# Kernel tuning notes

Hardware: AMD Instinct MI355X
Metric: run time of the kernel (lower is better)

## Reference

```python
import jax, jax.numpy as jnp
import numpy as np
import math

B, N, DIM = 2, 4096, 256
NUM_HEADS = 8
HEAD_DIM = DIM // NUM_HEADS
WINDOW = 7  # default window_size in create_local_mask


def local_mask(seq_len: int, window_size: int = WINDOW) -> jnp.ndarray:
    """Boolean [N,N] mask: True where attention is allowed (2D grid locality)."""
    grid = int(math.isqrt(seq_len))
    idx = jnp.arange(seq_len)
    row, col = idx // grid, idx % grid
    half = window_size // 2
    ok_row = jnp.abs(row[:, None] - row[None, :]) <= half
    ok_col = jnp.abs(col[:, None] - col[None, :]) <= half
    return ok_row & ok_col


def setup_inputs() -> dict:
    key = jax.random.key(0)
    k1, k2, k3, k4 = jax.random.split(key, 4)
    x = jax.random.normal(k1, (B, N, DIM), dtype=jnp.float32)
    W_qkv = jax.random.normal(k2, (3 * DIM, DIM), dtype=jnp.float32) * (DIM ** -0.5)
    W_proj = jax.random.normal(k3, (DIM, DIM), dtype=jnp.float32) * (DIM ** -0.5)
    b_proj = jax.random.normal(k4, (DIM,), dtype=jnp.float32) * 0.01
    temperature = jnp.ones((1,), dtype=jnp.float32)
    return {"x": x, "W_qkv": W_qkv, "W_proj": W_proj, "b_proj": b_proj,
            "temperature": temperature}


def reference(x, W_qkv, W_proj, b_proj, temperature):
    Bb, Nn, C = x.shape
    scale = HEAD_DIM ** -0.5
    # qkv linear (no bias): [B,N,3C] -> [3,B,H,N,hd]
    qkv = (x @ W_qkv.T).reshape(Bb, Nn, 3, NUM_HEADS, HEAD_DIM)
    qkv = jnp.transpose(qkv, (2, 0, 3, 1, 4))
    q, k, v = qkv[0], qkv[1], qkv[2]
    # scores with learnable temperature
    attn = jnp.einsum('bhqd,bhkd->bhqk', q, k) * (scale * temperature[0])
    mask = local_mask(Nn)  # training path: N > 100 -> mask applied
    attn = jnp.where(mask[None, None, :, :], attn, -jnp.inf)
    attn = jax.nn.softmax(attn, axis=-1)
    out = jnp.einsum('bhqk,bhkd->bhqd', attn, v)  # [B,H,N,hd]
    out = jnp.transpose(out, (0, 2, 1, 3)).reshape(Bb, Nn, C)
    return out @ W_proj.T + b_proj
```

## Files before the change

### kernel.cpp

```cpp
#include <hip/hip_runtime.h>
#include <hip/hip_bf16.h>
#include <hip/hip_fp16.h>
#include <math.h>

#define DIM   256
#define NHEAD 8
#define HD    32
#define NTOK  4096
#define GRD   64
#define BATCH 2
#define MTOT  (BATCH * NTOK)

typedef __attribute__((ext_vector_type(8))) short bf16x8;
typedef __attribute__((ext_vector_type(4))) float f32x4;
typedef _Float16 h8 __attribute__((ext_vector_type(8)));
typedef _Float16 h2v __attribute__((ext_vector_type(2)));

#if defined(__has_builtin)
#if __has_builtin(__builtin_amdgcn_fdot2)
#define HAVE_DOT2 1
#endif
#endif
#ifndef HAVE_DOT2
#define HAVE_DOT2 0
#endif

static __device__ __forceinline__ unsigned short f2b(float f) {
  __hip_bfloat16 h = __float2bfloat16(f);
  union { __hip_bfloat16 h; unsigned short u; } cv;
  cv.h = h;
  return cv.u;
}

__global__ __launch_bounds__(256) void cast3(const float* __restrict__ x,
                                             const float* __restrict__ wq,
                                             const float* __restrict__ wp,
                                             __hip_bfloat16* __restrict__ xb,
                                             __hip_bfloat16* __restrict__ wqb,
                                             __hip_bfloat16* __restrict__ wpb) {
  const int NX = (MTOT * DIM) / 4;
  const int NQ = (3 * DIM * DIM) / 4;
  const int NP = (DIM * DIM) / 4;
  int idx = blockIdx.x * 256 + threadIdx.x;
  if (idx >= NX + NQ + NP) return;
  const float* src;
  __hip_bfloat16* dst;
  int off;
  if (idx < NX)            { src = x;  dst = xb;  off = idx; }
  else if (idx < NX + NQ)  { src = wq; dst = wqb; off = idx - NX; }
  else                     { src = wp; dst = wpb; off = idx - NX - NQ; }
  float4 v = *(const float4*)&src[(size_t)off * 4];
  ushort4 o;
  o.x = f2b(v.x); o.y = f2b(v.y); o.z = f2b(v.z); o.w = f2b(v.w);
  *(ushort4*)&dst[(size_t)off * 4] = o;
}

template <int MODE>
__global__ __launch_bounds__(256) void gemm_bt(const __hip_bfloat16* __restrict__ A,
                                               const __hip_bfloat16* __restrict__ Bw,
                                               const float* __restrict__ bias,
                                               void* __restrict__ CoutV,
                                               int M, int N, int K) {
  __shared__ __hip_bfloat16 As[128 * 32];
  __shared__ __hip_bfloat16 Bs[128 * 32];
  const int tid = threadIdx.x;
  const int l = tid & 63, w = tid >> 6;
  const int bm = blockIdx.y * 128, bn = blockIdx.x * 128;
  const int wr = w >> 1, wc = w & 1;
  const int lr = l & 15, kh = l >> 4;

  f32x4 acc[4][4];
  #pragma unroll
  for (int i = 0; i < 4; ++i)
    #pragma unroll
    for (int j = 0; j < 4; ++j)
      acc[i][j] = (f32x4){0.f, 0.f, 0.f, 0.f};

  const int lrow = l >> 2;
  const int lcol = (l & 3) * 8;

  for (int k0 = 0; k0 < K; k0 += 32) {
    #pragma unroll
    for (int i = 0; i < 2; ++i) {
      const int r0 = (w * 2 + i) * 16;
      const __hip_bfloat16* ga = A  + (size_t)(bm + r0 + lrow) * K + k0 + lcol;
      const __hip_bfloat16* gb = Bw + (size_t)(bn + r0 + lrow) * K + k0 + lcol;
      __builtin_amdgcn_global_load_lds(
          (const __attribute__((address_space(1))) void*)ga,
          (__attribute__((address_space(3))) void*)&As[r0 * 32], 16, 0, 0);
      __builtin_amdgcn_global_load_lds(
          (const __attribute__((address_space(1))) void*)gb,
          (__attribute__((address_space(3))) void*)&Bs[r0 * 32], 16, 0, 0);
    }
    __syncthreads();

    bf16x8 af[4], bfr[4];
    #pragma unroll
    for (int f = 0; f < 4; ++f) {
      af[f]  = *(const bf16x8*)&As[(wr * 64 + f * 16 + lr) * 32 + kh * 8];
      bfr[f] = *(const bf16x8*)&Bs[(wc * 64 + f * 16 + lr) * 32 + kh * 8];
    }
    #pragma unroll
    for (int fi = 0; fi < 4; ++fi)
      #pragma unroll
      for (int fj = 0; fj < 4; ++fj)
        acc[fi][fj] = __builtin_amdgcn_mfma_f32_16x16x32_bf16(af[fi], bfr[fj], acc[fi][fj], 0, 0, 0);
    __syncthreads();
  }

  #pragma unroll
  for (int fi = 0; fi < 4; ++fi) {
    #pragma unroll
    for (int fj = 0; fj < 4; ++fj) {
      #pragma unroll
      for (int rr = 0; rr < 4; ++rr) {
        const int m = bm + wr * 64 + fi * 16 + kh * 4 + rr;
        const int n = bn + wc * 64 + fj * 16 + lr;
        const float v = acc[fi][fj][rr];
        if (MODE == 0) {
          ((float*)CoutV)[(size_t)m * N + n] = v + bias[n];
        } else {
          const int sel = n >> 8, rem = n & 255;
          const int hh = rem >> 5, d = rem & 31;
          const int bb = m >> 12, tok = m & 4095;
          ((_Float16*)CoutV)[((size_t)(sel * 16 + bb * 8 + hh) * NTOK + tok) * HD + d] =
              (_Float16)v;
        }
      }
    }
  }
}

__global__ __launch_bounds__(256) void local_attn(const _Float16* __restrict__ qkv,
                                                  const float* __restrict__ temp,
                                                  __hip_bfloat16* __restrict__ attn_out) {
  __shared__ _Float16 Ks[448 * 32];
  __shared__ _Float16 Vs[448 * 32];

  const int P = blockIdx.x;
  const int L = (P & 7) * 128 + (P >> 3);
  const int b = L >> 9, h = (L >> 6) & 7, r = L & 63;
  const int t = threadIdx.x;
  const int c = t >> 2, s = t & 3;

  const float scale = 0.17677669529663687f * temp[0];

  const _Float16* qplane = qkv + (size_t)(b * 8 + h) * (NTOK * HD);
  const _Float16* kplane = qkv + (size_t)(16 + b * 8 + h) * (NTOK * HD);
  const _Float16* vplane = qkv + (size_t)(32 + b * 8 + h) * (NTOK * HD);

  {
    const int jjl = (t & 3) ^ ((t >> 3) & 3);
    #pragma unroll
    for (int drp = 0; drp < 7; ++drp) {
      int rr = r - 3 + drp;
      rr = rr < 0 ? 0 : (rr > 63 ? 63 : rr);
      const int jj = jjl ^ (drp & 3);
      const _Float16* src = kplane + (size_t)rr * 2048 + (t >> 2) * 32 + jj * 8;
      const _Float16* srv = vplane + (size_t)rr * 2048 + (t >> 2) * 32 + jj * 8;
      const int w = t >> 6;
      __builtin_amdgcn_global_load_lds(
          (const __attribute__((address_space(1))) void*)src,
          (__attribute__((address_space(3))) void*)&Ks[(drp * 256 + w * 64) * 8], 16, 0, 0);
      __builtin_amdgcn_global_load_lds(
          (const __attribute__((address_space(1))) void*)srv,
          (__attribute__((address_space(3))) void*)&Vs[(drp * 256 + w * 64) * 8], 16, 0, 0);
    }
  }

  union { h8 v; h2v p[4]; } qu[4];
  {
    const _Float16* qr = qplane + (size_t)(r * GRD + c) * HD;
    #pragma unroll
    for (int jj = 0; jj < 4; ++jj) qu[jj].v = *(const h8*)&qr[jj * 8];
  }
  __syncthreads();

  const char* KB = (const char*)Ks;
  const char* VB = (const char*)Vs;
  float sc[14];
  int bs[14];
  float mx = -INFINITY;
  const int ndr = (s < 3) ? 2 : 1;
  #pragma unroll
  for (int i = 0; i < 2; ++i) {
    const int drp = s + i * 4;
    const int rr = r + drp - 3;
    const bool rowok = (i < ndr) && (rr >= 0) && (rr < GRD);
    #pragma unroll
    for (int dc = -3; dc <= 3; ++dc) {
      const int cc = c + dc;
      const bool ok = rowok && (cc >= 0) && (cc < GRD);
      int tk = drp * 64 + cc;
      tk = tk < 0 ? 0 : (tk > 447 ? 447 : tk);
      const int x = ((tk >> 1) ^ (tk >> 6)) & 3;
      const int sb = (tk << 6) ^ (x << 4);
      bs[i * 7 + dc + 3] = sb;
      float dot = 0.f;
      #pragma unroll
      for (int jj = 0; jj < 4; ++jj) {
        union { h8 v; h2v p[4]; } kk;
        kk.v = *(const h8*)(KB + (sb ^ (jj << 4)));
        #pragma unroll
        for (int kx = 0; kx < 4; ++kx) {
#if HAVE_DOT2
          dot = __builtin_amdgcn_fdot2(kk.p[kx], qu[jj].p[kx], dot, false);
#else
          dot = fmaf((float)kk.p[kx][0], (float)qu[jj].p[kx][0], dot);
          dot = fmaf((float)kk.p[kx][1], (float)qu[jj].p[kx][1], dot);
#endif
        }
      }
      const float v = ok ? dot * scale : -INFINITY;
      sc[i * 7 + dc + 3] = v;
      mx = fmaxf(mx, v);
    }
  }

  mx = fmaxf(mx, __shfl_xor(mx, 1));
  mx = fmaxf(mx, __shfl_xor(mx, 2));

  float psum = 0.f;
  #pragma unroll
  for (int i = 0; i < 14; ++i) {
    float e = __expf(sc[i] - mx);
    sc[i] = e;
    psum += e;
  }
  psum += __shfl_xor(psum, 1);
  psum += __shfl_xor(psum, 2);
  const float inv = 1.0f / psum;

  float o[HD];
  #pragma unroll
  for (int i = 0; i < HD; ++i) o[i] = 0.f;

  #pragma unroll
  for (int e = 0; e < 14; ++e) {
    const float p = sc[e];
    const int sb = bs[e];
    #pragma unroll
    for (int jj = 0; jj < 4; ++jj) {
      union { h8 v; h2v p2[4]; } vv;
      vv.v = *(const h8*)(VB + (sb ^ (jj << 4)));
      #pragma unroll
      for (int kx = 0; kx < 4; ++kx) {
        o[jj * 8 + kx * 2 + 0] = fmaf(p, (float)vv.p2[kx][0], o[jj * 8 + kx * 2 + 0]);
        o[jj * 8 + kx * 2 + 1] = fmaf(p, (float)vv.p2[kx][1], o[jj * 8 + kx * 2 + 1]);
      }
    }
  }

  #pragma unroll
  for (int d = 0; d < HD; ++d) {
    o[d] += __shfl_xor(o[d], 1);
    o[d] += __shfl_xor(o[d], 2);
  }

  union { uint4 u; unsigned short sh[8]; } pk;
  #pragma unroll
  for (int j = 0; j < 8; ++j) pk.sh[j] = f2b(o[s * 8 + j] * inv);
  __hip_bfloat16* dst = attn_out + ((size_t)(b * NTOK + r * GRD + c)) * DIM + h * HD + s * 8;
  *(uint4*)dst = pk.u;
}

extern "C" void kernel_launch(void* const* d_in, const int* in_sizes, int n_in,
                              void* d_out, int out_size, void* d_ws, size_t ws_size,
                              hipStream_t stream) {
  const float* x     = (const float*)d_in[0];
  const float* Wqkv  = (const float*)d_in[1];
  const float* Wproj = (const float*)d_in[2];
  const float* bproj = (const float*)d_in[3];
  const float* temp  = (const float*)d_in[4];
  float* out = (float*)d_out;

  char* ws = (char*)d_ws;
  _Float16* qkv_f16       = (_Float16*)ws;
  __hip_bfloat16* x_bf    = (__hip_bfloat16*)(ws + 25165824);
  __hip_bfloat16* attn_bf = (__hip_bfloat16*)(ws + 25165824);
  __hip_bfloat16* wq_bf   = (__hip_bfloat16*)(ws + 29360128);
  __hip_bfloat16* wp_bf   = (__hip_bfloat16*)(ws + 29753344);

  cast3<<<2304, 256, 0, stream>>>(x, Wqkv, Wproj, x_bf, wq_bf, wp_bf);

  {
    dim3 grid(3 * DIM / 128, MTOT / 128);
    gemm_bt<1><<<grid, 256, 0, stream>>>(x_bf, wq_bf, nullptr, qkv_f16,
                                         MTOT, 3 * DIM, DIM);
  }
  local_attn<<<BATCH * NHEAD * GRD, 256, 0, stream>>>(qkv_f16, temp, attn_bf);

  {
    dim3 grid(DIM / 128, MTOT / 128);
    gemm_bt<0><<<grid, 256, 0, stream>>>(attn_bf, wp_bf, bproj, out,
                                         MTOT, DIM, DIM);
  }
}
```

Before: 54.57 us.

## Fuse fp32-to-bf16 casts into GEMM loads and process two query rows per attention block

Removes the separate cast kernel. The GEMMs now load fp32 x and weights directly, convert them to bf16 in registers and store them to padded LDS tiles. The local attention kernel now handles two query rows per 512-thread block, so the 8 K/V rows it loads are shared across those two rows instead of loading 7 rows per single query row. This saves a launch and an intermediate round trip, but the GEMM loads become synchronous register loads rather than direct global-to-LDS transfers, and each GEMM block reads twice as many bytes from fp32 sources.

```diff
diff --git a/kernel.cpp b/kernel.cpp
--- a/kernel.cpp
+++ b/kernel.cpp
@@ -32,42 +32,25 @@
   return cv.u;
 }
 
-__global__ __launch_bounds__(256) void cast3(const float* __restrict__ x,
-                                             const float* __restrict__ wq,
-                                             const float* __restrict__ wp,
-                                             __hip_bfloat16* __restrict__ xb,
-                                             __hip_bfloat16* __restrict__ wqb,
-                                             __hip_bfloat16* __restrict__ wpb) {
-  const int NX = (MTOT * DIM) / 4;
-  const int NQ = (3 * DIM * DIM) / 4;
-  const int NP = (DIM * DIM) / 4;
-  int idx = blockIdx.x * 256 + threadIdx.x;
-  if (idx >= NX + NQ + NP) return;
-  const float* src;
-  __hip_bfloat16* dst;
-  int off;
-  if (idx < NX)            { src = x;  dst = xb;  off = idx; }
-  else if (idx < NX + NQ)  { src = wq; dst = wqb; off = idx - NX; }
-  else                     { src = wp; dst = wpb; off = idx - NX - NQ; }
-  float4 v = *(const float4*)&src[(size_t)off * 4];
-  ushort4 o;
-  o.x = f2b(v.x); o.y = f2b(v.y); o.z = f2b(v.z); o.w = f2b(v.w);
-  *(ushort4*)&dst[(size_t)off * 4] = o;
-}
-
-template <int MODE>
-__global__ __launch_bounds__(256) void gemm_bt(const __hip_bfloat16* __restrict__ A,
-                                               const __hip_bfloat16* __restrict__ Bw,
-                                               const float* __restrict__ bias,
-                                               void* __restrict__ CoutV,
-                                               int M, int N, int K) {
-  __shared__ __hip_bfloat16 As[128 * 32];
-  __shared__ __hip_bfloat16 Bs[128 * 32];
+static __device__ __forceinline__ bf16x8 pack8(float4 a0, float4 a1) {
+  union { bf16x8 v; unsigned short u[8]; } o;
+  o.u[0] = f2b(a0.x); o.u[1] = f2b(a0.y); o.u[2] = f2b(a0.z); o.u[3] = f2b(a0.w);
+  o.u[4] = f2b(a1.x); o.u[5] = f2b(a1.y); o.u[6] = f2b(a1.z); o.u[7] = f2b(a1.w);
+  return o.v;
+}
+
+__global__ __launch_bounds__(256) void gemm_qkv(const float* __restrict__ A,
+                                                const float* __restrict__ Bw,
+                                                _Float16* __restrict__ Cout) {
+  const int K = 256, N = 768;
+  __shared__ __hip_bfloat16 As[128 * 40];
+  __shared__ __hip_bfloat16 Bs[128 * 40];
   const int tid = threadIdx.x;
   const int l = tid & 63, w = tid >> 6;
   const int bm = blockIdx.y * 128, bn = blockIdx.x * 128;
   const int wr = w >> 1, wc = w & 1;
   const int lr = l & 15, kh = l >> 4;
+  const int lrow = l >> 2, lcol = (l & 3) * 8;
 
   f32x4 acc[4][4];
   #pragma unroll
@@ -76,21 +59,81 @@
     for (int j = 0; j < 4; ++j)
       acc[i][j] = (f32x4){0.f, 0.f, 0.f, 0.f};
 
-  const int lrow = l >> 2;
-  const int lcol = (l & 3) * 8;
-
   for (int k0 = 0; k0 < K; k0 += 32) {
     #pragma unroll
     for (int i = 0; i < 2; ++i) {
       const int r0 = (w * 2 + i) * 16;
-      const __hip_bfloat16* ga = A  + (size_t)(bm + r0 + lrow) * K + k0 + lcol;
-      const __hip_bfloat16* gb = Bw + (size_t)(bn + r0 + lrow) * K + k0 + lcol;
+      const float* ga = A  + (size_t)(bm + r0 + lrow) * K + k0 + lcol;
+      const float* gb = Bw + (size_t)(bn + r0 + lrow) * K + k0 + lcol;
+      float4 a0 = *(const float4*)ga, a1 = *(const float4*)(ga + 4);
+      float4 b0 = *(const float4*)gb, b1 = *(const float4*)(gb + 4);
+      *(bf16x8*)&As[(r0 + lrow) * 40 + lcol] = pack8(a0, a1);
+      *(bf16x8*)&Bs[(r0 + lrow) * 40 + lcol] = pack8(b0, b1);
+    }
+    __syncthreads();
+
+    bf16x8 af[4], bfr[4];
+    #pragma unroll
+    for (int f = 0; f < 4; ++f) {
+      af[f]  = *(const bf16x8*)&As[(wr * 64 + f * 16 + lr) * 40 + kh * 8];
+      bfr[f] = *(const bf16x8*)&Bs[(wc * 64 + f * 16 + lr) * 40 + kh * 8];
+    }
+    #pragma unroll
+    for (int fi = 0; fi < 4; ++fi)
+      #pragma unroll
+      for (int fj = 0; fj < 4; ++fj)
+        acc[fi][fj] = __builtin_amdgcn_mfma_f32_16x16x32_bf16(af[fi], bfr[fj], acc[fi][fj], 0, 0, 0);
+    __syncthreads();
+  }
+
+  #pragma unroll
+  for (int fi = 0; fi < 4; ++fi)
+    #pragma unroll
+    for (int fj = 0; fj < 4; ++fj)
+      #pragma unroll
+      for (int rr = 0; rr < 4; ++rr) {
+        const int m = bm + wr * 64 + fi * 16 + kh * 4 + rr;
+        const int n = bn + wc * 64 + fj * 16 + lr;
+        const int sel = n >> 8, rem = n & 255;
+        const int hh = rem >> 5, d = rem & 31;
+        const int bb = m >> 12, tok = m & 4095;
+        Cout[((size_t)(sel * 16 + bb * 8 + hh) * NTOK + tok) * HD + d] =
+            (_Float16)acc[fi][fj][rr];
+      }
+}
+
+__global__ __launch_bounds__(256) void gemm_proj(const __hip_bfloat16* __restrict__ A,
+                                                 const float* __restrict__ Bw,
+                                                 const float* __restrict__ bias,
+                                                 float* __restrict__ Cout) {
+  const int K = 256, N = 256;
+  __shared__ __hip_bfloat16 As[128 * 32];
+  __shared__ __hip_bfloat16 Bs[128 * 40];
+  const int tid = threadIdx.x;
+  const int l = tid & 63, w = tid >> 6;
+  const int bm = blockIdx.y * 128, bn = blockIdx.x * 128;
+  const int wr = w >> 1, wc = w & 1;
+  const int lr = l & 15, kh = l >> 4;
+  const int lrow = l >> 2, lcol = (l & 3) * 8;
+
+  f32x4 acc[4][4];
+  #pragma unroll
+  for (int i = 0; i < 4; ++i)
+    #pragma unroll
+    for (int j = 0; j < 4; ++j)
+      acc[i][j] = (f32x4){0.f, 0.f, 0.f, 0.f};
+
+  for (int k0 = 0; k0 < K; k0 += 32) {
+    #pragma unroll
+    for (int i = 0; i < 2; ++i) {
+      const int r0 = (w * 2 + i) * 16;
+      const __hip_bfloat16* ga = A + (size_t)(bm + r0 + lrow) * K + k0 + lcol;
       __builtin_amdgcn_global_load_lds(
           (const __attribute__((address_space(1))) void*)ga,
           (__attribute__((address_space(3))) void*)&As[r0 * 32], 16, 0, 0);
-      __builtin_amdgcn_global_load_lds(
-          (const __attribute__((address_space(1))) void*)gb,
-          (__attribute__((address_space(3))) void*)&Bs[r0 * 32], 16, 0, 0);
+      const float* gb = Bw + (size_t)(bn + r0 + lrow) * K + k0 + lcol;
+      float4 b0 = *(const float4*)gb, b1 = *(const float4*)(gb + 4);
+      *(bf16x8*)&Bs[(r0 + lrow) * 40 + lcol] = pack8(b0, b1);
     }
     __syncthreads();
 
@@ -98,7 +141,7 @@
     #pragma unroll
     for (int f = 0; f < 4; ++f) {
       af[f]  = *(const bf16x8*)&As[(wr * 64 + f * 16 + lr) * 32 + kh * 8];
-      bfr[f] = *(const bf16x8*)&Bs[(wc * 64 + f * 16 + lr) * 32 + kh * 8];
+      bfr[f] = *(const bf16x8*)&Bs[(wc * 64 + f * 16 + lr) * 40 + kh * 8];
     }
     #pragma unroll
     for (int fi = 0; fi < 4; ++fi)
@@ -109,39 +152,30 @@
   }
 
   #pragma unroll
-  for (int fi = 0; fi < 4; ++fi) {
-    #pragma unroll
-    for (int fj = 0; fj < 4; ++fj) {
+  for (int fi = 0; fi < 4; ++fi)
+    #pragma unroll
+    for (int fj = 0; fj < 4; ++fj)
       #pragma unroll
       for (int rr = 0; rr < 4; ++rr) {
         const int m = bm + wr * 64 + fi * 16 + kh * 4 + rr;
         const int n = bn + wc * 64 + fj * 16 + lr;
-        const float v = acc[fi][fj][rr];
-        if (MODE == 0) {
-          ((float*)CoutV)[(size_t)m * N + n] = v + bias[n];
-        } else {
-          const int sel = n >> 8, rem = n & 255;
-          const int hh = rem >> 5, d = rem & 31;
-          const int bb = m >> 12, tok = m & 4095;
-          ((_Float16*)CoutV)[((size_t)(sel * 16 + bb * 8 + hh) * NTOK + tok) * HD + d] =
-              (_Float16)v;
-        }
+        Cout[(size_t)m * N + n] = acc[fi][fj][rr] + bias[n];
       }
-    }
-  }
-}
-
-__global__ __launch_bounds__(256) void local_attn(const _Float16* __restrict__ qkv,
+}
+
+__global__ __launch_bounds__(512) void local_attn(const _Float16* __restrict__ qkv,
                                                   const float* __restrict__ temp,
                                                   __hip_bfloat16* __restrict__ attn_out) {
-  __shared__ _Float16 Ks[448 * 32];
-  __shared__ _Float16 Vs[448 * 32];
+  __shared__ _Float16 Ks[512 * 32];
+  __shared__ _Float16 Vs[512 * 32];
 
   const int P = blockIdx.x;
-  const int L = (P & 7) * 128 + (P >> 3);
-  const int b = L >> 9, h = (L >> 6) & 7, r = L & 63;
+  const int L = (P & 7) * 64 + (P >> 3);
+  const int plane = L >> 5, rp = L & 31;
+  const int b = plane >> 3, h = plane & 7;
   const int t = threadIdx.x;
-  const int c = t >> 2, s = t & 3;
+  const int qr = t >> 8, c = (t >> 2) & 63, s = t & 3;
+  const int r = rp * 2 + qr;
 
   const float scale = 0.17677669529663687f * temp[0];
 
@@ -150,29 +184,35 @@
   const _Float16* vplane = qkv + (size_t)(32 + b * 8 + h) * (NTOK * HD);
 
   {
-    const int jjl = (t & 3) ^ ((t >> 3) & 3);
-    #pragma unroll
-    for (int drp = 0; drp < 7; ++drp) {
-      int rr = r - 3 + drp;
-      rr = rr < 0 ? 0 : (rr > 63 ? 63 : rr);
-      const int jj = jjl ^ (drp & 3);
-      const _Float16* src = kplane + (size_t)rr * 2048 + (t >> 2) * 32 + jj * 8;
-      const _Float16* srv = vplane + (size_t)rr * 2048 + (t >> 2) * 32 + jj * 8;
-      const int w = t >> 6;
+    const int rbase = rp * 2 - 3;
+    const int wbase = t & ~63;
+    #pragma unroll
+    for (int i = 0; i < 4; ++i) {
+      const int id = i * 512 + t;
+      const int drp = id >> 8;
+      const int tokloc = (id >> 2) & 63;
+      const int jjp = id & 3;
+      const int x = ((tokloc >> 1) ^ drp) & 3;
+      const int jj = jjp ^ x;
+      int row = rbase + drp;
+      row = row < 0 ? 0 : (row > 63 ? 63 : row);
+      const _Float16* src = kplane + (size_t)row * 2048 + tokloc * 32 + jj * 8;
+      const _Float16* srv = vplane + (size_t)row * 2048 + tokloc * 32 + jj * 8;
+      const int dbase = (i * 512 + wbase) * 8;
       __builtin_amdgcn_global_load_lds(
           (const __attribute__((address_space(1))) void*)src,
-          (__attribute__((address_space(3))) void*)&Ks[(drp * 256 + w * 64) * 8], 16, 0, 0);
+          (__attribute__((address_space(3))) void*)&Ks[dbase], 16, 0, 0);
       __builtin_amdgcn_global_load_lds(
           (const __attribute__((address_space(1))) void*)srv,
-          (__attribute__((address_space(3))) void*)&Vs[(drp * 256 + w * 64) * 8], 16, 0, 0);
+          (__attribute__((address_space(3))) void*)&Vs[dbase], 16, 0, 0);
     }
   }
 
   union { h8 v; h2v p[4]; } qu[4];
   {
-    const _Float16* qr = qplane + (size_t)(r * GRD + c) * HD;
-    #pragma unroll
-    for (int jj = 0; jj < 4; ++jj) qu[jj].v = *(const h8*)&qr[jj * 8];
+    const _Float16* qrp_ = qplane + (size_t)(r * GRD + c) * HD;
+    #pragma unroll
+    for (int jj = 0; jj < 4; ++jj) qu[jj].v = *(const h8*)&qrp_[jj * 8];
   }
   __syncthreads();
 
@@ -184,15 +224,16 @@
   const int ndr = (s < 3) ? 2 : 1;
   #pragma unroll
   for (int i = 0; i < 2; ++i) {
-    const int drp = s + i * 4;
-    const int rr = r + drp - 3;
+    const int dr = s - 3 + 4 * i;
+    const int drp = dr + 3 + qr;
+    const int rr = r + dr;
     const bool rowok = (i < ndr) && (rr >= 0) && (rr < GRD);
     #pragma unroll
     for (int dc = -3; dc <= 3; ++dc) {
       const int cc = c + dc;
       const bool ok = rowok && (cc >= 0) && (cc < GRD);
       int tk = drp * 64 + cc;
-      tk = tk < 0 ? 0 : (tk > 447 ? 447 : tk);
+      tk = tk < 0 ? 0 : (tk > 511 ? 511 : tk);
       const int x = ((tk >> 1) ^ (tk >> 6)) & 3;
       const int sb = (tk << 6) ^ (x << 4);
       bs[i * 7 + dc + 3] = sb;
@@ -276,23 +317,16 @@
 
   char* ws = (char*)d_ws;
   _Float16* qkv_f16       = (_Float16*)ws;
-  __hip_bfloat16* x_bf    = (__hip_bfloat16*)(ws + 25165824);
   __hip_bfloat16* attn_bf = (__hip_bfloat16*)(ws + 25165824);
-  __hip_bfloat16* wq_bf   = (__hip_bfloat16*)(ws + 29360128);
-  __hip_bfloat16* wp_bf   = (__hip_bfloat16*)(ws + 29753344);
-
-  cast3<<<2304, 256, 0, stream>>>(x, Wqkv, Wproj, x_bf, wq_bf, wp_bf);
 
   {
     dim3 grid(3 * DIM / 128, MTOT / 128);
-    gemm_bt<1><<<grid, 256, 0, stream>>>(x_bf, wq_bf, nullptr, qkv_f16,
-                                         MTOT, 3 * DIM, DIM);
-  }
-  local_attn<<<BATCH * NHEAD * GRD, 256, 0, stream>>>(qkv_f16, temp, attn_bf);
+    gemm_qkv<<<grid, 256, 0, stream>>>(x, Wqkv, qkv_f16);
+  }
+  local_attn<<<BATCH * NHEAD * (GRD / 2), 512, 0, stream>>>(qkv_f16, temp, attn_bf);
 
   {
     dim3 grid(DIM / 128, MTOT / 128);
-    gemm_bt<0><<<grid, 256, 0, stream>>>(attn_bf, wp_bf, bproj, out,
-                                         MTOT, DIM, DIM);
-  }
-}
+    gemm_proj<<<grid, 256, 0, stream>>>(attn_bf, Wproj, bproj, out);
+  }
+}
```

New measurement: 49.79 us. 8.8% less time.
